# Performance work log

Measured on AMD Instinct MI355X. Metric: run time of the kernel, lower is better.

Reference implementation:

```python
import jax, jax.numpy as jnp
import numpy as np

B, CIN, COUT, H, W, K, G = 2, 256, 256, 128, 128, 3, 4
PAD = (K - 1) // 2


def setup_inputs() -> dict:
    key = jax.random.key(0)
    k1, k2, k3, k4 = jax.random.split(key, 4)
    x = jax.random.normal(k1, (B, CIN, H, W), dtype=jnp.float32)
    # conv_offset: 1x1 conv, out channels = G*2*K*K. (Zero-init in the module; use
    # small random weights so offsets are non-trivial for correctness testing.)
    w_offset = jax.random.normal(k2, (G * 2 * K * K, CIN), dtype=jnp.float32) * 0.01
    b_offset = jax.random.normal(k3, (G * 2 * K * K,), dtype=jnp.float32) * 0.5
    # DeformConv weight (bias=False in mmcv DeformConv)
    w_deform = jax.random.normal(k4, (COUT, CIN, K, K), dtype=jnp.float32) * (1.0 / np.sqrt(CIN * K * K))
    return {"x": x, "w_offset": w_offset, "b_offset": b_offset, "w_deform": w_deform}


def _bilinear_gather(img, y, x):
    """img: [B,G,Cg,H,W]; y,x: [B,G,H,W] float sample coords -> [B,G,Cg,H,W].
    Zero padding outside the image (mmcv DCN bilinear semantics)."""
    b, g, cg, h, w = img.shape
    imgf = img.reshape(b, g, cg, h * w)
    y0 = jnp.floor(y)
    x0 = jnp.floor(x)
    out = jnp.zeros((b, g, cg, h * w), img.dtype)
    for yy, xx in ((y0, x0), (y0, x0 + 1.0), (y0 + 1.0, x0), (y0 + 1.0, x0 + 1.0)):
        wgt = (1.0 - jnp.abs(y - yy)) * (1.0 - jnp.abs(x - xx))
        valid = (yy >= 0) & (yy < h) & (xx >= 0) & (xx < w)
        wgt = jnp.where(valid, wgt, 0.0)
        yi = jnp.clip(yy, 0, h - 1).astype(jnp.int32)
        xi = jnp.clip(xx, 0, w - 1).astype(jnp.int32)
        idx = (yi * w + xi).reshape(b, g, 1, h * w)
        vals = jnp.take_along_axis(imgf, jnp.broadcast_to(idx, (b, g, cg, h * w)), axis=3)
        out = out + wgt.reshape(b, g, 1, h * w) * vals
    return out.reshape(b, g, cg, h, w)


def reference(x, w_offset, b_offset, w_deform):
    b, cin, h, w = x.shape
    cout, _, k, _ = w_deform.shape
    pad = (k - 1) // 2
    # 1x1 offset conv
    offset = jnp.einsum('bchw,oc->bohw', x, w_offset) + b_offset[None, :, None, None]
    g = offset.shape[1] // (2 * k * k)
    off = offset.reshape(b, g, k * k, 2, h, w)  # (dy, dx) per kernel tap, mmcv layout
    xg = x.reshape(b, g, cin // g, h, w)
    hh = jnp.arange(h, dtype=x.dtype)[:, None]
    ww = jnp.arange(w, dtype=x.dtype)[None, :]
    out = jnp.zeros((b, cout, h, w), x.dtype)
    for i in range(k):
        for j in range(k):
            t = i * k + j
            ys = hh - pad + i + off[:, :, t, 0]  # [B,G,H,W]
            xs = ww - pad + j + off[:, :, t, 1]
            samp = _bilinear_gather(xg, ys, xs).reshape(b, cin, h, w)
            out = out + jnp.einsum('bchw,oc->bohw', samp, w_deform[:, :, i, j])
    return jax.nn.relu(out)
```

## Files before the change

kernel.cpp:

```cpp
#include <hip/hip_runtime.h>
#include <stdint.h>

#define HW    16384
#define CIN   256
#define COUT  256
#define Hh    128
#define Ww    128
#define OFFC  72

typedef __attribute__((ext_vector_type(4))) float    f32x4;
typedef __attribute__((ext_vector_type(2))) _Float16 f16x2;
typedef __attribute__((ext_vector_type(8))) _Float16 f16x8;
typedef unsigned short u16;
typedef unsigned int   u32;

__device__ __forceinline__ u16 f2h(float f) { return __builtin_bit_cast(u16, (_Float16)f); }
__device__ __forceinline__ u32 pk2(float f) { u32 h = f2h(f); return h | (h << 16); }
__device__ __forceinline__ f16x2 bch(u32 u) { return __builtin_bit_cast(f16x2, u); }

__device__ __forceinline__ void bar_nodrain() {
  asm volatile("s_waitcnt lgkmcnt(0)" ::: "memory");
  __builtin_amdgcn_sched_barrier(0);
  __builtin_amdgcn_s_barrier();
  __builtin_amdgcn_sched_barrier(0);
}

__global__ __launch_bounds__(256) void kprep(const float* __restrict__ x, const float* __restrict__ wd,
                                             const float* __restrict__ wo, u16* __restrict__ xt,
                                             u16* __restrict__ wfrag, u16* __restrict__ wfrag2) {
  __shared__ float smem[64 * 129];
  int blk = blockIdx.x;
  if (blk < 1024) {
    int bg = blk >> 7;
    int p0 = (blk & 127) << 7;
    const float* src = x + (size_t)bg * 64 * HW + p0;
    #pragma unroll
    for (int r = 0; r < 8; ++r) {
      int idx = (threadIdx.x + 256 * r) * 4;
      int c = idx >> 7, px = idx & 127;
      f32x4 v = *(const f32x4*)(src + (size_t)c * HW + px);
      smem[c * 129 + px + 0] = v[0];
      smem[c * 129 + px + 1] = v[1];
      smem[c * 129 + px + 2] = v[2];
      smem[c * 129 + px + 3] = v[3];
    }
    __syncthreads();
    u16* dstb = xt + ((size_t)bg * HW + p0) * 64;
    #pragma unroll
    for (int k = 0; k < 4; ++k) {
      int e  = k * 256 + threadIdx.x;
      int px = e >> 3, ck = e & 7;
      u32 w[4];
      #pragma unroll
      for (int m = 0; m < 4; ++m) {
        float lo = smem[(ck * 8 + 2 * m + 0) * 129 + px];
        float hi = smem[(ck * 8 + 2 * m + 1) * 129 + px];
        w[m] = (u32)f2h(lo) | ((u32)f2h(hi) << 16);
      }
      *(uint4*)(dstb + (size_t)e * 8) = make_uint4(w[0], w[1], w[2], w[3]);
    }
  } else if (blk < 1152) {
    int bb = blk - 1024;
    int nh = bb & 31;
    int g  = bb >> 5;
    const float* src = wd + (size_t)(nh * 8) * 2304 + (size_t)g * 64 * 9;
    #pragma unroll
    for (int r = 0; r < 18; ++r) {
      int idx = threadIdx.x + 256 * r;
      int cl  = idx / 576;
      int rem = idx - cl * 576;
      smem[cl * 576 + rem] = src[(size_t)cl * 2304 + rem];
    }
    __syncthreads();
    int nt = nh >> 1, nb = (nh & 1) * 8;
    #pragma unroll
    for (int r = 0; r < 18; ++r) {
      int o  = threadIdx.x + 256 * r;
      int j  = o & 7;
      int n8 = (o >> 3) & 7;
      int q  = (o >> 6) & 3;
      int kcl = o >> 8;
      int t = kcl >> 1, half = kcl & 1;
      int cg = half * 32 + q * 8 + j;
      float v = smem[n8 * 576 + cg * 9 + t];
      int kc = (g * 9 + t) * 2 + half;
      int lane = q * 16 + nb + n8;
      wfrag[((size_t)(kc * 16 + nt) * 64 + lane) * 8 + j] = f2h(v);
    }
  } else {
    int e = (blk - 1152) * 256 + threadIdx.x;
    int j = e & 7;
    int lane = (e >> 3) & 63;
    int idx = e >> 9;
    int kc = idx / 5, nt = idx - 5 * kc;
    int n16 = lane & 15, q = lane >> 4;
    int oc = nt * 16 + n16;
    int c  = kc * 32 + q * 8 + j;
    float v = (oc < OFFC) ? wo[(size_t)oc * CIN + c] : 0.f;
    wfrag2[e] = f2h(v);
  }
}

__device__ __forceinline__ void mkpre(float yy, float xx, int* ob, u32* wp) {
  float y0f = floorf(yy), x0f = floorf(xx);
  float fy = yy - y0f, fx = xx - x0f;
  int y0 = (int)y0f, x0 = (int)x0f;
  int y1 = y0 + 1, x1 = x0 + 1;
  float vy0 = (y0 >= 0 && y0 < Hh) ? 1.f : 0.f;
  float vy1 = (y1 >= 0 && y1 < Hh) ? 1.f : 0.f;
  float vx0 = (x0 >= 0 && x0 < Ww) ? 1.f : 0.f;
  float vx1 = (x1 >= 0 && x1 < Ww) ? 1.f : 0.f;
  wp[0] = pk2((1.f - fy) * (1.f - fx) * vy0 * vx0);
  wp[1] = pk2((1.f - fy) * fx * vy0 * vx1);
  wp[2] = pk2(fy * (1.f - fx) * vy1 * vx0);
  wp[3] = pk2(fy * fx * vy1 * vx1);
  int cy0 = min(max(y0, 0), Hh - 1), cy1 = min(max(y1, 0), Hh - 1);
  int cx0 = min(max(x0, 0), Ww - 1), cx1 = min(max(x1, 0), Ww - 1);
  ob[0] = (cy0 * Ww + cx0) << 7;
  ob[1] = (cy0 * Ww + cx1) << 7;
  ob[2] = (cy1 * Ww + cx0) << 7;
  ob[3] = (cy1 * Ww + cx1) << 7;
}

__device__ __forceinline__ uint4 bil16(const uint4* v, const u32* wp) {
  f16x2 W0 = bch(wp[0]), W1 = bch(wp[1]), W2 = bch(wp[2]), W3 = bch(wp[3]);
  uint4 r;
  { f16x2 s = bch(v[0].x) * W0 + bch(v[1].x) * W1 + bch(v[2].x) * W2 + bch(v[3].x) * W3; r.x = __builtin_bit_cast(u32, s); }
  { f16x2 s = bch(v[0].y) * W0 + bch(v[1].y) * W1 + bch(v[2].y) * W2 + bch(v[3].y) * W3; r.y = __builtin_bit_cast(u32, s); }
  { f16x2 s = bch(v[0].z) * W0 + bch(v[1].z) * W1 + bch(v[2].z) * W2 + bch(v[3].z) * W3; r.z = __builtin_bit_cast(u32, s); }
  { f16x2 s = bch(v[0].w) * W0 + bch(v[1].w) * W1 + bch(v[2].w) * W2 + bch(v[3].w) * W3; r.w = __builtin_bit_cast(u32, s); }
  return r;
}

__global__ __launch_bounds__(512) void k2(const u16* __restrict__ xt, const u16* __restrict__ wfrag2,
                                          const float* __restrict__ bo, const u16* __restrict__ wfrag,
                                          float* __restrict__ out) {
  __shared__ u16   astage[2 * 8 * 512];
  __shared__ float offl[64 * 74];
  int tid  = threadIdx.x;
  int lane = tid & 63, n16 = lane & 15, q = (tid >> 4) & 3;
  int wv   = tid >> 6;
  int sp   = wv >> 1;
  int hp   = wv & 1;
  int b  = blockIdx.x >> 8;
  int p0 = (blockIdx.x & 255) << 6;
  int h  = p0 >> 7, w0 = p0 & 127;
  const char* xtb = (const char*)xt + (size_t)b * 4 * HW * 128;
  float fh  = (float)h;
  float fxp = (float)(w0 + sp * 16 + n16);
  int   chb = hp * 64 + q * 16;

  f32x4 acc[4][2];
  #pragma unroll
  for (int mt = 0; mt < 4; ++mt) {
    acc[mt][0] = (f32x4){0.f, 0.f, 0.f, 0.f};
    acc[mt][1] = (f32x4){0.f, 0.f, 0.f, 0.f};
  }

  if (wv < 4) {
    f32x4 oacc[5];
    #pragma unroll
    for (int nt = 0; nt < 5; ++nt) {
      int oc = nt * 16 + n16;
      float bv = (oc < OFFC) ? bo[oc] : 0.f;
      oacc[nt] = (f32x4){bv, bv, bv, bv};
    }
    #pragma unroll
    for (int kc = 0; kc < 8; ++kc) {
      int g = kc >> 1;
      f16x8 af = __builtin_bit_cast(f16x8, *(const uint4*)(xtb +
          ((size_t)(g * HW + p0 + wv * 16 + n16)) * 128 + (kc & 1) * 64 + q * 16));
      #pragma unroll
      for (int nt = 0; nt < 5; ++nt) {
        f16x8 bfo = __builtin_bit_cast(f16x8, *(const uint4*)(wfrag2 + (size_t)(((kc * 5 + nt) << 6) + lane) * 8));
        oacc[nt] = __builtin_amdgcn_mfma_f32_16x16x32_f16(af, bfo, oacc[nt], 0, 0, 0);
      }
    }
    #pragma unroll
    for (int nt = 0; nt < 5; ++nt) {
      int oc = nt * 16 + n16;
      if (oc < OFFC) {
        #pragma unroll
        for (int r = 0; r < 4; ++r)
          offl[(wv * 16 + q * 4 + r) * 74 + oc] = oacc[nt][r];
      }
    }
  }
  uint4 bf0[2];
  bf0[0] = *(const uint4*)(wfrag + ((size_t)(wv * 2 + 0) * 64 + lane) * 8);
  bf0[1] = *(const uint4*)(wfrag + ((size_t)(wv * 2 + 1) * 64 + lane) * 8);
  __syncthreads();

  uint4 dA[4], dB[4];
  u32   wpA[4], wpB[4];

  auto issue = [&](int gt, uint4* dd, u32* wpp) {
    int pxl = sp * 16 + n16;
    float oy = offl[pxl * 74 + gt * 2];
    float ox = offl[pxl * 74 + gt * 2 + 1];
    int g = (gt * 57) >> 9;
    int t = gt - g * 9;
    int i = (t * 683) >> 11;
    int j = t - i * 3;
    int ob[4];
    mkpre(fh + (float)(i - 1) + oy, fxp + (float)(j - 1) + ox, ob, wpp);
    const char* xg = xtb + (size_t)g * HW * 128;
    #pragma unroll
    for (int c = 0; c < 4; ++c)
      dd[c] = *(const uint4*)(xg + ob[c] + chb);
  };
  auto consume = [&](int slot, int gt) {
    uint4 bf1[2];
    const u16* wb1 = wfrag + ((size_t)((2 * gt + 1) * 16 + wv * 2) * 64 + lane) * 8;
    bf1[0] = *(const uint4*)(wb1);
    bf1[1] = *(const uint4*)(wb1 + 512);
    __builtin_amdgcn_s_setprio(1);
    #pragma unroll
    for (int mt = 0; mt < 4; ++mt) {
      f16x8 af = __builtin_bit_cast(f16x8,
          *(const uint4*)&astage[(slot * 8 + mt * 2 + 0) * 512 + lane * 8]);
      acc[mt][0] = __builtin_amdgcn_mfma_f32_16x16x32_f16(af, __builtin_bit_cast(f16x8, bf0[0]), acc[mt][0], 0, 0, 0);
      acc[mt][1] = __builtin_amdgcn_mfma_f32_16x16x32_f16(af, __builtin_bit_cast(f16x8, bf0[1]), acc[mt][1], 0, 0, 0);
    }
    #pragma unroll
    for (int mt = 0; mt < 4; ++mt) {
      f16x8 af = __builtin_bit_cast(f16x8,
          *(const uint4*)&astage[(slot * 8 + mt * 2 + 1) * 512 + lane * 8]);
      acc[mt][0] = __builtin_amdgcn_mfma_f32_16x16x32_f16(af, __builtin_bit_cast(f16x8, bf1[0]), acc[mt][0], 0, 0, 0);
      acc[mt][1] = __builtin_amdgcn_mfma_f32_16x16x32_f16(af, __builtin_bit_cast(f16x8, bf1[1]), acc[mt][1], 0, 0, 0);
    }
    __builtin_amdgcn_s_setprio(0);
    if (gt < 35) {
      const u16* wb0 = wfrag + ((size_t)((2 * gt + 2) * 16 + wv * 2) * 64 + lane) * 8;
      bf0[0] = *(const uint4*)(wb0);
      bf0[1] = *(const uint4*)(wb0 + 512);
    }
  };

  issue(0, dA, wpA);
  issue(1, dB, wpB);
  *(uint4*)&astage[(0 * 8 + sp * 2 + hp) * 512 + lane * 8] = bil16(dA, wpA);
  bar_nodrain();

  #pragma unroll 1
  for (int gt = 0; gt < 36; gt += 2) {
    *(uint4*)&astage[(1 * 8 + sp * 2 + hp) * 512 + lane * 8] = bil16(dB, wpB);
    if (gt + 2 < 36) issue(gt + 2, dA, wpA);
    consume(0, gt);
    bar_nodrain();
    if (gt + 2 < 36) {
      *(uint4*)&astage[(0 * 8 + sp * 2 + hp) * 512 + lane * 8] = bil16(dA, wpA);
      issue(gt + 3, dB, wpB);
    }
    consume(1, gt + 1);
    bar_nodrain();
  }

  float* op = out + (size_t)b * COUT * HW + p0;
  #pragma unroll
  for (int mt = 0; mt < 4; ++mt)
    #pragma unroll
    for (int j = 0; j < 2; ++j) {
      f32x4 v = acc[mt][j];
      #pragma unroll
      for (int r = 0; r < 4; ++r) v[r] = fmaxf(v[r], 0.f);
      int cout = wv * 32 + j * 16 + n16;
      *(f32x4*)(op + (size_t)cout * HW + mt * 16 + q * 4) = v;
    }
}

extern "C" void kernel_launch(void* const* d_in, const int* in_sizes, int n_in,
                              void* d_out, int out_size, void* d_ws, size_t ws_size,
                              hipStream_t stream) {
  const float* x  = (const float*)d_in[0];
  const float* wo = (const float*)d_in[1];
  const float* bo = (const float*)d_in[2];
  const float* wd = (const float*)d_in[3];
  float* out = (float*)d_out;

  u16* xtp    = (u16*)d_ws;
  u16* wfrag  = (u16*)((char*)d_ws + 16777216);
  u16* wfrag2 = (u16*)((char*)d_ws + 16777216 + 1179648);

  kprep<<<1232, 256, 0, stream>>>(x, wd, wo, xtp, wfrag, wfrag2);
  k2   <<<512,  512, 0, stream>>>(xtp, wfrag2, bo, wfrag, out);
}
```

Before: 198.2 us.

## Double-buffer weight fragments, swizzle blocks, and simplify input transpose

The main kernel now keeps two register sets of B-fragments (all four per tap) and prefetches the next tap's weights at the start of each consume, instead of loading half of them inside consume. It also swizzles the block index to spread neighbouring tiles across dies/XCDs, adds a launch bound requesting two blocks per CU, drops the sched_barriers and setprio, and rewrites the prep transpose to convert directly from global loads without going through LDS. These aim to hide weight-load latency and cut prep-kernel overhead, at the cost of more registers, which could cause spills under the tighter occupancy bound.

```diff
diff --git a/kernel.cpp b/kernel.cpp
--- a/kernel.cpp
+++ b/kernel.cpp
@@ -18,47 +18,36 @@
 __device__ __forceinline__ u32 pk2(float f) { u32 h = f2h(f); return h | (h << 16); }
 __device__ __forceinline__ f16x2 bch(u32 u) { return __builtin_bit_cast(f16x2, u); }
 
-__device__ __forceinline__ void bar_nodrain() {
+__device__ __forceinline__ void bar() {
   asm volatile("s_waitcnt lgkmcnt(0)" ::: "memory");
-  __builtin_amdgcn_sched_barrier(0);
   __builtin_amdgcn_s_barrier();
-  __builtin_amdgcn_sched_barrier(0);
+  asm volatile("" ::: "memory");
 }
 
 __global__ __launch_bounds__(256) void kprep(const float* __restrict__ x, const float* __restrict__ wd,
                                              const float* __restrict__ wo, u16* __restrict__ xt,
                                              u16* __restrict__ wfrag, u16* __restrict__ wfrag2) {
-  __shared__ float smem[64 * 129];
+  __shared__ float smem[8 * 576];
   int blk = blockIdx.x;
   if (blk < 1024) {
     int bg = blk >> 7;
     int p0 = (blk & 127) << 7;
-    const float* src = x + (size_t)bg * 64 * HW + p0;
-    #pragma unroll
-    for (int r = 0; r < 8; ++r) {
-      int idx = (threadIdx.x + 256 * r) * 4;
-      int c = idx >> 7, px = idx & 127;
-      f32x4 v = *(const f32x4*)(src + (size_t)c * HW + px);
-      smem[c * 129 + px + 0] = v[0];
-      smem[c * 129 + px + 1] = v[1];
-      smem[c * 129 + px + 2] = v[2];
-      smem[c * 129 + px + 3] = v[3];
-    }
-    __syncthreads();
-    u16* dstb = xt + ((size_t)bg * HW + p0) * 64;
-    #pragma unroll
-    for (int k = 0; k < 4; ++k) {
-      int e  = k * 256 + threadIdx.x;
-      int px = e >> 3, ck = e & 7;
-      u32 w[4];
+    int pq = threadIdx.x & 31;
+    int ck = threadIdx.x >> 5;
+    const float* src = x + (size_t)bg * 64 * HW + p0 + pq * 4;
+    u32 pk[4][4];
+    #pragma unroll
+    for (int m = 0; m < 4; ++m) {
+      f32x4 lo = *(const f32x4*)(src + (size_t)(ck * 8 + 2 * m + 0) * HW);
+      f32x4 hi = *(const f32x4*)(src + (size_t)(ck * 8 + 2 * m + 1) * HW);
       #pragma unroll
-      for (int m = 0; m < 4; ++m) {
-        float lo = smem[(ck * 8 + 2 * m + 0) * 129 + px];
-        float hi = smem[(ck * 8 + 2 * m + 1) * 129 + px];
-        w[m] = (u32)f2h(lo) | ((u32)f2h(hi) << 16);
-      }
-      *(uint4*)(dstb + (size_t)e * 8) = make_uint4(w[0], w[1], w[2], w[3]);
-    }
+      for (int j = 0; j < 4; ++j)
+        pk[j][m] = (u32)f2h(lo[j]) | ((u32)f2h(hi[j]) << 16);
+    }
+    u16* dst = xt + ((size_t)bg * HW + p0 + pq * 4) * 64 + ck * 8;
+    #pragma unroll
+    for (int j = 0; j < 4; ++j)
+      *(uint4*)(dst + (size_t)j * 64) = make_uint4(pk[j][0], pk[j][1], pk[j][2], pk[j][3]);
   } else if (blk < 1152) {
     int bb = blk - 1024;
     int nh = bb & 31;
@@ -132,9 +121,9 @@
   return r;
 }
 
-__global__ __launch_bounds__(512) void k2(const u16* __restrict__ xt, const u16* __restrict__ wfrag2,
-                                          const float* __restrict__ bo, const u16* __restrict__ wfrag,
-                                          float* __restrict__ out) {
+__global__ __launch_bounds__(512, 2) void k2(const u16* __restrict__ xt, const u16* __restrict__ wfrag2,
+                                             const float* __restrict__ bo, const u16* __restrict__ wfrag,
+                                             float* __restrict__ out) {
   __shared__ u16   astage[2 * 8 * 512];
   __shared__ float offl[64 * 74];
   int tid  = threadIdx.x;
@@ -142,19 +131,31 @@
   int wv   = tid >> 6;
   int sp   = wv >> 1;
   int hp   = wv & 1;
-  int b  = blockIdx.x >> 8;
-  int p0 = (blockIdx.x & 255) << 6;
+  int blk  = blockIdx.x;
+  int swz  = (blk & 7) * 64 + (blk >> 3);
+  int b  = swz >> 8;
+  int p0 = (swz & 255) << 6;
   int h  = p0 >> 7, w0 = p0 & 127;
   const char* xtb = (const char*)xt + (size_t)b * 4 * HW * 128;
   float fh  = (float)h;
   float fxp = (float)(w0 + sp * 16 + n16);
   int   chb = hp * 64 + q * 16;
+  int   pxl = sp * 16 + n16;
 
   f32x4 acc[4][2];
   #pragma unroll
   for (int mt = 0; mt < 4; ++mt) {
     acc[mt][0] = (f32x4){0.f, 0.f, 0.f, 0.f};
     acc[mt][1] = (f32x4){0.f, 0.f, 0.f, 0.f};
+  }
+
+  uint4 bfA[4], bfB[4];
+  {
+    const u16* wb = wfrag + ((size_t)(2 * wv) * 64 + lane) * 8;
+    bfA[0] = *(const uint4*)(wb);
+    bfA[1] = *(const uint4*)(wb + 512);
+    bfA[2] = *(const uint4*)(wb + 8192);
+    bfA[3] = *(const uint4*)(wb + 8704);
   }
 
   if (wv < 4) {
@@ -186,16 +187,12 @@
       }
     }
   }
-  uint4 bf0[2];
-  bf0[0] = *(const uint4*)(wfrag + ((size_t)(wv * 2 + 0) * 64 + lane) * 8);
-  bf0[1] = *(const uint4*)(wfrag + ((size_t)(wv * 2 + 1) * 64 + lane) * 8);
   __syncthreads();
 
   uint4 dA[4], dB[4];
   u32   wpA[4], wpB[4];
 
   auto issue = [&](int gt, uint4* dd, u32* wpp) {
-    int pxl = sp * 16 + n16;
     float oy = offl[pxl * 74 + gt * 2];
     float ox = offl[pxl * 74 + gt * 2 + 1];
     int g = (gt * 57) >> 9;
@@ -209,51 +206,47 @@
     for (int c = 0; c < 4; ++c)
       dd[c] = *(const uint4*)(xg + ob[c] + chb);
   };
-  auto consume = [&](int slot, int gt) {
-    uint4 bf1[2];
-    const u16* wb1 = wfrag + ((size_t)((2 * gt + 1) * 16 + wv * 2) * 64 + lane) * 8;
-    bf1[0] = *(const uint4*)(wb1);
-    bf1[1] = *(const uint4*)(wb1 + 512);
-    __builtin_amdgcn_s_setprio(1);
+  auto consume = [&](int slot, int gt, uint4* bfC, uint4* bfN) {
+    if (gt < 35) {
+      const u16* wb = wfrag + ((size_t)((2 * (gt + 1)) * 16 + 2 * wv) * 64 + lane) * 8;
+      bfN[0] = *(const uint4*)(wb);
+      bfN[1] = *(const uint4*)(wb + 512);
+      bfN[2] = *(const uint4*)(wb + 8192);
+      bfN[3] = *(const uint4*)(wb + 8704);
+    }
     #pragma unroll
     for (int mt = 0; mt < 4; ++mt) {
       f16x8 af = __builtin_bit_cast(f16x8,
           *(const uint4*)&astage[(slot * 8 + mt * 2 + 0) * 512 + lane * 8]);
-      acc[mt][0] = __builtin_amdgcn_mfma_f32_16x16x32_f16(af, __builtin_bit_cast(f16x8, bf0[0]), acc[mt][0], 0, 0, 0);
-      acc[mt][1] = __builtin_amdgcn_mfma_f32_16x16x32_f16(af, __builtin_bit_cast(f16x8, bf0[1]), acc[mt][1], 0, 0, 0);
+      acc[mt][0] = __builtin_amdgcn_mfma_f32_16x16x32_f16(af, __builtin_bit_cast(f16x8, bfC[0]), acc[mt][0], 0, 0, 0);
+      acc[mt][1] = __builtin_amdgcn_mfma_f32_16x16x32_f16(af, __builtin_bit_cast(f16x8, bfC[1]), acc[mt][1], 0, 0, 0);
     }
     #pragma unroll
     for (int mt = 0; mt < 4; ++mt) {
       f16x8 af = __builtin_bit_cast(f16x8,
           *(const uint4*)&astage[(slot * 8 + mt * 2 + 1) * 512 + lane * 8]);
-      acc[mt][0] = __builtin_amdgcn_mfma_f32_16x16x32_f16(af, __builtin_bit_cast(f16x8, bf1[0]), acc[mt][0], 0, 0, 0);
-      acc[mt][1] = __builtin_amdgcn_mfma_f32_16x16x32_f16(af, __builtin_bit_cast(f16x8, bf1[1]), acc[mt][1], 0, 0, 0);
-    }
-    __builtin_amdgcn_s_setprio(0);
-    if (gt < 35) {
-      const u16* wb0 = wfrag + ((size_t)((2 * gt + 2) * 16 + wv * 2) * 64 + lane) * 8;
-      bf0[0] = *(const uint4*)(wb0);
-      bf0[1] = *(const uint4*)(wb0 + 512);
+      acc[mt][0] = __builtin_amdgcn_mfma_f32_16x16x32_f16(af, __builtin_bit_cast(f16x8, bfC[2]), acc[mt][0], 0, 0, 0);
+      acc[mt][1] = __builtin_amdgcn_mfma_f32_16x16x32_f16(af, __builtin_bit_cast(f16x8, bfC[3]), acc[mt][1], 0, 0, 0);
     }
   };
 
   issue(0, dA, wpA);
   issue(1, dB, wpB);
   *(uint4*)&astage[(0 * 8 + sp * 2 + hp) * 512 + lane * 8] = bil16(dA, wpA);
-  bar_nodrain();
+  bar();
 
   #pragma unroll 1
   for (int gt = 0; gt < 36; gt += 2) {
     *(uint4*)&astage[(1 * 8 + sp * 2 + hp) * 512 + lane * 8] = bil16(dB, wpB);
     if (gt + 2 < 36) issue(gt + 2, dA, wpA);
-    consume(0, gt);
-    bar_nodrain();
+    consume(0, gt, bfA, bfB);
+    bar();
     if (gt + 2 < 36) {
       *(uint4*)&astage[(0 * 8 + sp * 2 + hp) * 512 + lane * 8] = bil16(dA, wpA);
       issue(gt + 3, dB, wpB);
     }
-    consume(1, gt + 1);
-    bar_nodrain();
+    consume(1, gt + 1, bfB, bfA);
+    bar();
   }
 
   float* op = out + (size_t)b * COUT * HW + p0;
```

Result: no change. 196.6 us (-0.8%).
